# Kernel optimization log

Hardware: AMD Instinct MI355X
Metric: run time of the kernel (lower is better)

Reference implementation:

```python
import jax, jax.numpy as jnp
import numpy as np

N_NODES = 100000
N_EDGES = 1600000
D_IN, D_HID, D_OUT = 128, 256, 128


def _sage_conv(x, src, dst, W_l, b_l, W_r, num_nodes):
    """PyG SAGEConv with mean aggregation: lin_l(mean_j x_j) + lin_r(x_i)."""
    msg = x[src]                                              # [E, d] gather
    agg = jax.ops.segment_sum(msg, dst, num_segments=num_nodes)   # [N, d]
    cnt = jax.ops.segment_sum(jnp.ones((src.shape[0],), x.dtype), dst,
                              num_segments=num_nodes)         # [N]
    agg = agg / jnp.maximum(cnt, 1.0)[:, None]                # mean (0 for isolated)
    return agg @ W_l + b_l + x @ W_r


def setup_inputs() -> dict:
    key = jax.random.key(0)
    ks = jax.random.split(key, 8)
    x = jax.random.normal(ks[0], (N_NODES, D_IN), dtype=jnp.float32)
    edge_index = jax.random.randint(ks[1], (2, N_EDGES), 0, N_NODES, dtype=jnp.int64)
    perturb_first = jax.random.normal(ks[2], (N_NODES, D_HID), dtype=jnp.float32) * 0.05
    perturb_last = jax.random.normal(ks[3], (N_NODES, D_OUT), dtype=jnp.float32) * 0.05
    s1 = 1.0 / np.sqrt(D_IN)
    s2 = 1.0 / np.sqrt(D_HID)
    return {
        "x": x,
        "edge_index": edge_index,
        "perturb_first": perturb_first,
        "perturb_last": perturb_last,
        "Wl1": jax.random.normal(ks[4], (D_IN, D_HID), dtype=jnp.float32) * s1,
        "bl1": jnp.zeros((D_HID,), dtype=jnp.float32),
        "Wr1": jax.random.normal(ks[5], (D_IN, D_HID), dtype=jnp.float32) * s1,
        "Wl2": jax.random.normal(ks[6], (D_HID, D_OUT), dtype=jnp.float32) * s2,
        "bl2": jnp.zeros((D_OUT,), dtype=jnp.float32),
        "Wr2": jax.random.normal(ks[7], (D_HID, D_OUT), dtype=jnp.float32) * s2,
    }


def reference(x, edge_index, perturb_first, perturb_last,
              Wl1, bl1, Wr1, Wl2, bl2, Wr2):
    # PyG default flow source_to_target: messages from edge_index[0] -> edge_index[1]
    src, dst = edge_index[0], edge_index[1]
    n = x.shape[0]
    # forward() only applies model[0] and model[3] (the two SAGEConvs);
    # the LayerNorm/PReLU entries in the Sequential are skipped.
    h = _sage_conv(x, src, dst, Wl1, bl1, Wr1, n) + perturb_first
    out = _sage_conv(h, src, dst, Wl2, bl2, Wr2, n) + perturb_last
    return out
```

## Files before the change

### kernel.cpp

```cpp
#include <hip/hip_runtime.h>

#define N_NODES 100000
#define N_EDGES 1600000
#define NBUCK 196
#define CAP_BIN 64
#define CAP_B 12288
#define CVT_BLKS 12500

typedef float v4f __attribute__((ext_vector_type(4)));
typedef __bf16 v8bf __attribute__((ext_vector_type(8)));
typedef __bf16 v4bf __attribute__((ext_vector_type(4)));
typedef unsigned int v4u __attribute__((ext_vector_type(4)));

union FragU { v4u u; v8bf b; };
union PkU { unsigned int u; __bf16 h[2]; };
union Pk2 { uint2 u2; __bf16 h[4]; };

__device__ __forceinline__ int clampN(int v) {
    return v < 0 ? 0 : (v >= N_NODES ? N_NODES - 1 : v);
}
__device__ __forceinline__ float bfhi(unsigned int u) { return __uint_as_float(u & 0xffff0000u); }
__device__ __forceinline__ float bflo(unsigned int u) { return __uint_as_float(u << 16); }

__device__ __forceinline__ void gll16(const void* g, void* l) {
    __builtin_amdgcn_global_load_lds(
        (const __attribute__((address_space(1))) unsigned int*)g,
        (__attribute__((address_space(3))) unsigned int*)l, 16, 0, 0);
}

__global__ __launch_bounds__(256) void k_prep(
    const float* __restrict__ x, __bf16* __restrict__ a2,
    const float* __restrict__ Wl1, const float* __restrict__ Wr1,
    const float* __restrict__ Wl2, const float* __restrict__ Wr2,
    __bf16* __restrict__ Wl1p, __bf16* __restrict__ Wr1p,
    __bf16* __restrict__ Wl2p, __bf16* __restrict__ Wr2p,
    const int* __restrict__ dst, int* __restrict__ bucketCnt)
{
    const int b = blockIdx.x, tid = threadIdx.x;
    if (b < CVT_BLKS) {
        int t = b * 256 + tid;
        float4 v = ((const float4*)x)[t];
        int row = t >> 5, c4 = t & 31;
        v4bf o = { (__bf16)v.x, (__bf16)v.y, (__bf16)v.z, (__bf16)v.w };
        *(v4bf*)(a2 + (size_t)row * 256 + 128 + c4 * 4) = o;
    } else if (b < CVT_BLKS + 64) {
        int pb = b - CVT_BLKS;
        int which = pb >> 4;
        int t = (pb & 15) * 256 + tid;
        const float* W = which == 0 ? Wl1 : which == 1 ? Wr1 : which == 2 ? Wl2 : Wr2;
        __bf16* Wp     = which == 0 ? Wl1p : which == 1 ? Wr1p : which == 2 ? Wl2p : Wr2p;
        const int N = (which < 2) ? 256 : 128;
        const int NT = N >> 4;
        int l = t & 63;
        int fi = t >> 6;
        int kc = fi / NT, nt = fi % NT;
        int k0 = kc * 32 + (l >> 4) * 8;
        int col = nt * 16 + (l & 15);
        v8bf o;
        #pragma unroll
        for (int j = 0; j < 8; ++j) o[j] = (__bf16)W[(size_t)(k0 + j) * N + col];
        *(v8bf*)(Wp + (size_t)t * 8) = o;
    } else {
        __shared__ int h[NBUCK];
        for (int i = tid; i < NBUCK; i += 256) h[i] = 0;
        __syncthreads();
        int cb = b - CVT_BLKS - 64;
        int e0 = cb * 4096;
        int e1 = e0 + 4096; if (e1 > N_EDGES) e1 = N_EDGES;
        for (int e = e0 + tid; e < e1; e += 256)
            atomicAdd(&h[clampN(dst[e]) >> 9], 1);
        __syncthreads();
        for (int i = tid; i < NBUCK; i += 256)
            if (h[i]) atomicAdd(&bucketCnt[i], h[i]);
    }
}

__global__ __launch_bounds__(256) void k_scanb(
    const int* __restrict__ bucketCnt, int* __restrict__ baseB,
    int* __restrict__ gcur, int* __restrict__ rowp)
{
    const int t = threadIdx.x;
    int v = (t < NBUCK) ? bucketCnt[t] : 0;
    int incl = v;
    #pragma unroll
    for (int off = 1; off < 64; off <<= 1) {
        int u = __shfl_up(incl, off);
        if ((t & 63) >= off) incl += u;
    }
    __shared__ int wt[4];
    if ((t & 63) == 63) wt[t >> 6] = incl;
    __syncthreads();
    int woff = 0;
    #pragma unroll
    for (int k = 0; k < 4; ++k) if (k < (t >> 6)) woff += wt[k];
    int excl = woff + incl - v;
    if (t < NBUCK) { baseB[t] = excl; gcur[t] = excl; }
    if (t == NBUCK) { baseB[NBUCK] = excl; rowp[N_NODES] = excl; }
}

__global__ __launch_bounds__(256) void k_bin(
    const int* __restrict__ src, const int* __restrict__ dst,
    int* __restrict__ gcur, unsigned int* __restrict__ packed)
{
    __shared__ unsigned int bins[256 * CAP_BIN];
    __shared__ int cnt[256];
    const int tid = threadIdx.x;
    cnt[tid] = 0;
    __syncthreads();
    const int epb = (N_EDGES + gridDim.x - 1) / gridDim.x;
    int e0 = blockIdx.x * epb;
    int e1 = e0 + epb; if (e1 > N_EDGES) e1 = N_EDGES;
    for (int ch = e0; ch < e1; ch += 4096) {
        int chEnd = ch + 4096; if (chEnd > e1) chEnd = e1;
        for (int e = ch + tid; e < chEnd; e += 256) {
            int s = clampN(src[e]);
            int d = clampN(dst[e]);
            unsigned int val = (unsigned int)s | ((unsigned int)(d & 511) << 17);
            int b = d >> 9;
            int slot = atomicAdd(&cnt[b], 1);
            if (slot < CAP_BIN) bins[b * CAP_BIN + slot] = val;
            else {
                int g = atomicAdd(&gcur[b], 1);
                packed[g] = val;
            }
        }
        __syncthreads();
        int n = cnt[tid]; if (n > CAP_BIN) n = CAP_BIN;
        if (tid < NBUCK && n > 0) {
            int g = atomicAdd(&gcur[tid], n);
            for (int j = 0; j < n; ++j) packed[g + j] = bins[tid * CAP_BIN + j];
        }
        __syncthreads();
        cnt[tid] = 0;
        __syncthreads();
    }
}

__global__ __launch_bounds__(256) void k_bucket(
    const int* __restrict__ baseB, const unsigned int* __restrict__ packed,
    int* __restrict__ rowp, int* __restrict__ edge_src)
{
    __shared__ int hist[512], cur[512];
    __shared__ int wt[4];
    __shared__ unsigned int buf[CAP_B];
    const int b = blockIdx.x, tid = threadIdx.x;
    const int lo = baseB[b], hi = baseB[b + 1], c = hi - lo;
    for (int i = tid; i < 512; i += 256) hist[i] = 0;
    __syncthreads();
    for (int e = tid; e < c; e += 256)
        atomicAdd(&hist[packed[lo + e] >> 17], 1);
    __syncthreads();
    int a0 = hist[2 * tid], a1 = hist[2 * tid + 1];
    int s = a0 + a1;
    int incl = s;
    #pragma unroll
    for (int off = 1; off < 64; off <<= 1) {
        int u = __shfl_up(incl, off);
        if ((tid & 63) >= off) incl += u;
    }
    if ((tid & 63) == 63) wt[tid >> 6] = incl;
    __syncthreads();
    int woff = 0;
    #pragma unroll
    for (int k = 0; k < 4; ++k) if (k < (tid >> 6)) woff += wt[k];
    int ep = woff + incl - s;
    cur[2 * tid] = ep;
    cur[2 * tid + 1] = ep + a0;
    int n0 = b * 512 + 2 * tid;
    if (n0 < N_NODES)     rowp[n0]     = lo + ep;
    if (n0 + 1 < N_NODES) rowp[n0 + 1] = lo + ep + a0;
    __syncthreads();
    for (int e = tid; e < c; e += 256) {
        unsigned int v = packed[lo + e];
        int dl = v >> 17;
        unsigned int sv = v & 0x1FFFFu;
        int pos = atomicAdd(&cur[dl], 1);
        if (pos < CAP_B) buf[pos] = sv;
        else edge_src[lo + pos] = (int)sv;
    }
    __syncthreads();
    int cc = c < CAP_B ? c : CAP_B;
    for (int e = tid; e < cc; e += 256) edge_src[lo + e] = (int)buf[e];
}

template<int MODE>
__global__ __launch_bounds__(256) void k_gather16(
    const int* __restrict__ rp, const int* __restrict__ es,
    const __bf16* __restrict__ tab, void* __restrict__ outp)
{
    int wid = (blockIdx.x * 256 + threadIdx.x) >> 6;
    int l = threadIdx.x & 63;
    if (wid >= N_NODES) return;
    int start = rp[wid], end = rp[wid + 1];
    const int slot = l >> 4, c = l & 15;
    const size_t coff = (MODE == 0) ? (size_t)(128 + c * 8) : (size_t)(c * 8);
    float s0 = 0.f, s1 = 0.f, s2 = 0.f, s3 = 0.f;
    float s4 = 0.f, s5 = 0.f, s6 = 0.f, s7 = 0.f;

    int e0 = start + slot;
    int e1 = e0 + 4;
    int e2 = e1 + 4;
    bool h0 = e0 < end, h1 = e1 < end, h2 = e2 < end;
    v4u r0 = {0, 0, 0, 0}, r1 = {0, 0, 0, 0};
    if (h0) r0 = *(const v4u*)(tab + (size_t)es[e0] * 256 + coff);
    if (h1) r1 = *(const v4u*)(tab + (size_t)es[e1] * 256 + coff);
    int i2 = h2 ? es[e2] : 0;

    while (h0) {
        v4u r2 = {0, 0, 0, 0};
        if (h2) r2 = *(const v4u*)(tab + (size_t)i2 * 256 + coff);
        int e3 = e2 + 4;
        bool h3 = e3 < end;
        int i3 = h3 ? es[e3] : 0;
        s0 += bflo(r0.x); s1 += bfhi(r0.x);
        s2 += bflo(r0.y); s3 += bfhi(r0.y);
        s4 += bflo(r0.z); s5 += bfhi(r0.z);
        s6 += bflo(r0.w); s7 += bfhi(r0.w);
        r0 = r1; r1 = r2;
        h0 = h1; h1 = h2; h2 = h3;
        i2 = i3; e2 = e3;
    }

    s0 += __shfl_xor(s0, 16); s1 += __shfl_xor(s1, 16);
    s2 += __shfl_xor(s2, 16); s3 += __shfl_xor(s3, 16);
    s4 += __shfl_xor(s4, 16); s5 += __shfl_xor(s5, 16);
    s6 += __shfl_xor(s6, 16); s7 += __shfl_xor(s7, 16);
    s0 += __shfl_xor(s0, 32); s1 += __shfl_xor(s1, 32);
    s2 += __shfl_xor(s2, 32); s3 += __shfl_xor(s3, 32);
    s4 += __shfl_xor(s4, 32); s5 += __shfl_xor(s5, 32);
    s6 += __shfl_xor(s6, 32); s7 += __shfl_xor(s7, 32);
    float invd = 1.f / fmaxf((float)(end - start), 1.f);
    if (slot == 0) {
        if (MODE == 0) {
            PkU a, b, cc, d;
            a.h[0] = (__bf16)(s0 * invd); a.h[1] = (__bf16)(s1 * invd);
            b.h[0] = (__bf16)(s2 * invd); b.h[1] = (__bf16)(s3 * invd);
            cc.h[0] = (__bf16)(s4 * invd); cc.h[1] = (__bf16)(s5 * invd);
            d.h[0] = (__bf16)(s6 * invd); d.h[1] = (__bf16)(s7 * invd);
            v4u o = { a.u, b.u, cc.u, d.u };
            ((v4u*)outp)[(size_t)wid * 32 + c] = o;
        } else {
            v4u pu = *(const v4u*)(tab + (size_t)wid * 256 + 128 + c * 8);
            float4 va, vb;
            va.x = s0 * invd + bflo(pu.x); va.y = s1 * invd + bfhi(pu.x);
            va.z = s2 * invd + bflo(pu.y); va.w = s3 * invd + bfhi(pu.y);
            vb.x = s4 * invd + bflo(pu.z); vb.y = s5 * invd + bfhi(pu.z);
            vb.z = s6 * invd + bflo(pu.w); vb.w = s7 * invd + bfhi(pu.w);
            ((float4*)outp)[(size_t)wid * 32 + c * 2]     = va;
            ((float4*)outp)[(size_t)wid * 32 + c * 2 + 1] = vb;
        }
    }
}

template<int LAYER>
__device__ __forceinline__ void stage_a32(
    const __bf16* __restrict__ A, int tile, int tid, char* buf)
{
    const int row0 = tile * 32;
    #pragma unroll
    for (int k = 0; k < 2; ++k) {
        int ch = k * 512 + tid;
        int row = ch >> 5, c16 = ch & 31;
        int sc = c16 ^ (row & 7);
        gll16(A + (size_t)(row0 + row) * 256 + sc * 8, buf + ch * 16);
    }
}

template<int LAYER>
__device__ __forceinline__ void stage_p32(
    const float* __restrict__ pert, int tile, int tid, char* pS)
{
    const int row0 = tile * 32;
    if (LAYER == 1) {
        #pragma unroll
        for (int k = 0; k < 4; ++k) {
            int ch = k * 512 + tid;
            int row = ch >> 6, c16 = ch & 63;
            gll16(pert + (size_t)(row0 + row) * 256 + c16 * 4, pS + ch * 16);
        }
    } else {
        #pragma unroll
        for (int k = 0; k < 2; ++k) {
            int ch = k * 512 + tid;
            int row = ch >> 5, c16 = ch & 31;
            gll16(pert + (size_t)(row0 + row) * 128 + c16 * 4, pS + ch * 16);
        }
    }
}

template<int LAYER>
__global__ __launch_bounds__(512, 2) void k_gws(
    const __bf16* __restrict__ A,
    const __bf16* __restrict__ WpA, const __bf16* __restrict__ WpB,
    const float* __restrict__ bias, const float* __restrict__ pert,
    __bf16* __restrict__ outb, int ntiles)
{
    __shared__ char aS0[16384];
    __shared__ char aS1[16384];
    __shared__ char hS[16384];
    __shared__ char pS[(LAYER == 1) ? 32768 : 16384];
    const int tid = threadIdx.x;
    const int w = tid >> 6, l = tid & 63;
    const int lrow = l & 15, kg = l >> 4;
    const v4f zf = {0.f, 0.f, 0.f, 0.f};

    FragU bw[8][2];
    #pragma unroll
    for (int kc = 0; kc < 8; ++kc)
        #pragma unroll
        for (int nt = 0; nt < 2; ++nt) {
            const __bf16* Wp;
            int fi;
            if (LAYER == 1) {
                Wp = (kc < 4) ? WpA : WpB;
                fi = (kc & 3) * 16 + w * 2 + nt;
            } else {
                Wp = (w < 4) ? WpA : WpB;
                fi = kc * 8 + (w & 3) * 2 + nt;
            }
            bw[kc][nt].u = *(const v4u*)(Wp + ((size_t)fi * 64 + l) * 8);
        }

    int tile = blockIdx.x;
    int cur = 0;
    if (tile < ntiles) stage_a32<LAYER>(A, tile, tid, aS0);
    __syncthreads();

    for (; tile < ntiles; tile += gridDim.x) {
        stage_p32<LAYER>(pert, tile, tid, pS);
        int nxt = tile + (int)gridDim.x;
        if (nxt < ntiles)
            stage_a32<LAYER>(A, nxt, tid, cur ? aS0 : aS1);
        const char* aSc = cur ? aS1 : aS0;

        const int row0 = tile * 32;
        #pragma unroll
        for (int rf = 0; rf < 2; ++rf) {
            const int arow = rf * 16 + lrow;
            FragU a[8];
            #pragma unroll
            for (int kc = 0; kc < 8; ++kc) {
                int byte = arow * 512 + ((kc * 64 + kg * 16) ^ ((arow & 7) << 4));
                a[kc].u = *(const v4u*)(aSc + byte);
            }
            v4f acc[2] = {zf, zf};
            #pragma unroll
            for (int kc = 0; kc < 8; ++kc) {
                acc[0] = __builtin_amdgcn_mfma_f32_16x16x32_bf16(a[kc].b, bw[kc][0].b, acc[0], 0, 0, 0);
                acc[1] = __builtin_amdgcn_mfma_f32_16x16x32_bf16(a[kc].b, bw[kc][1].b, acc[1], 0, 0, 0);
            }
            #pragma unroll
            for (int nt = 0; nt < 2; ++nt)
                #pragma unroll
                for (int r = 0; r < 4; ++r) {
                    int row = rf * 16 + kg * 4 + r;
                    int col = w * 32 + nt * 16 + lrow;
                    int byte = (row * 512 + col * 2) ^ ((row & 7) << 4);
                    *(__bf16*)(hS + byte) = (__bf16)acc[nt][r];
                }
        }
        __syncthreads();

        #pragma unroll
        for (int it = 0; it < 4; ++it) {
            int chunk = it * 512 + tid;
            int row = chunk >> 6, c4 = chunk & 63;
            int grow = row0 + row;
            int byte = (row * 512 + c4 * 8) ^ ((row & 7) << 4);
            Pk2 pk; pk.u2 = *(const uint2*)(hS + byte);
            if (LAYER == 1) {
                float4 pv = *(const float4*)(pS + (row * 64 + c4) * 16);
                float4 bv = ((const float4*)bias)[c4];
                PkU o0, o1;
                o0.h[0] = (__bf16)((float)pk.h[0] + pv.x + bv.x);
                o0.h[1] = (__bf16)((float)pk.h[1] + pv.y + bv.y);
                o1.h[0] = (__bf16)((float)pk.h[2] + pv.z + bv.z);
                o1.h[1] = (__bf16)((float)pk.h[3] + pv.w + bv.w);
                uint2 ov = { o0.u, o1.u };
                *(uint2*)(outb + (size_t)grow * 256 + c4 * 4) = ov;
            } else {
                uint2 ov;
                if (c4 < 32) {
                    ov = pk.u2;
                } else {
                    float4 pv = *(const float4*)(pS + (row * 32 + (c4 - 32)) * 16);
                    float4 bv = ((const float4*)bias)[c4 - 32];
                    PkU o0, o1;
                    o0.h[0] = (__bf16)((float)pk.h[0] + pv.x + bv.x);
                    o0.h[1] = (__bf16)((float)pk.h[1] + pv.y + bv.y);
                    o1.h[0] = (__bf16)((float)pk.h[2] + pv.z + bv.z);
                    o1.h[1] = (__bf16)((float)pk.h[3] + pv.w + bv.w);
                    ov.x = o0.u; ov.y = o1.u;
                }
                *(uint2*)(outb + (size_t)grow * 256 + c4 * 4) = ov;
            }
        }
        __syncthreads();
        cur ^= 1;
    }
}

extern "C" void kernel_launch(void* const* d_in, const int* in_sizes, int n_in,
                              void* d_out, int out_size, void* d_ws, size_t ws_size,
                              hipStream_t stream)
{
    const float* x   = (const float*)d_in[0];
    const int*   ei  = (const int*)d_in[1];
    const float* p1  = (const float*)d_in[2];
    const float* p2  = (const float*)d_in[3];
    const float* Wl1 = (const float*)d_in[4];
    const float* bl1 = (const float*)d_in[5];
    const float* Wr1 = (const float*)d_in[6];
    const float* Wl2 = (const float*)d_in[7];
    const float* bl2 = (const float*)d_in[8];
    const float* Wr2 = (const float*)d_in[9];
    const int* src = ei;
    const int* dst = ei + N_EDGES;

    const size_t NPAD = (size_t)N_NODES + 64;
    char* wp = (char*)d_ws;
    __bf16* a2   = (__bf16*)wp; wp += NPAD * 256 * 2;
    __bf16* hb   = (__bf16*)wp; wp += NPAD * 256 * 2;
    __bf16* u2b  = (__bf16*)wp; wp += NPAD * 256 * 2;
    __bf16* Wl1p = (__bf16*)wp; wp += 128 * 256 * 2;
    __bf16* Wr1p = (__bf16*)wp; wp += 128 * 256 * 2;
    __bf16* Wl2p = (__bf16*)wp; wp += 256 * 128 * 2;
    __bf16* Wr2p = (__bf16*)wp; wp += 256 * 128 * 2;
    int* bucketCnt = (int*)wp; wp += 512 * 4;
    int* baseB     = (int*)wp; wp += 512 * 4;
    int* gcur      = (int*)wp; wp += 512 * 4;
    int* rowp      = (int*)wp; wp += (size_t)(N_NODES + 1) * 4 + 12;
    unsigned int* packed = (unsigned int*)wp; wp += (size_t)N_EDGES * 4;
    int* es        = (int*)wp;

    hipMemsetAsync(bucketCnt, 0, 512 * 4, stream);

    const int gblocks = (N_NODES * 64 + 255) / 256;
    const int tiles32 = N_NODES / 32;
    const int prep_blocks = CVT_BLKS + 64 + (N_EDGES + 4095) / 4096;

    k_prep<<<prep_blocks, 256, 0, stream>>>(
        x, a2, Wl1, Wr1, Wl2, Wr2, Wl1p, Wr1p, Wl2p, Wr2p, dst, bucketCnt);
    k_scanb<<<1, 256, 0, stream>>>(bucketCnt, baseB, gcur, rowp);
    k_bin<<<256, 256, 0, stream>>>(src, dst, gcur, packed);
    k_bucket<<<NBUCK, 256, 0, stream>>>(baseB, packed, rowp, es);

    k_gather16<0><<<gblocks, 256, 0, stream>>>(rowp, es, a2, a2);
    k_gws<1><<<512, 512, 0, stream>>>(a2, Wl1p, Wr1p, bl1, p1, hb, tiles32);
    k_gws<2><<<512, 512, 0, stream>>>(hb, Wl2p, Wr2p, bl2, p2, u2b, tiles32);
    k_gather16<1><<<gblocks, 256, 0, stream>>>(rowp, es, u2b, (void*)d_out);
}
```

Before: 289.4 us.

## Fuse layer-1 neighbor mean aggregation into the layer-1 GEMM kernel

The standalone layer-1 gather kernel is removed, and each 32-row tile of the layer-1 GEMM now gathers and averages its own neighbor rows straight into shared memory before running the MFMA products. This avoids writing the aggregated bf16 features to global memory and reading them back, and drops one kernel launch. In exchange, the GEMM kernel loses its double-buffered prefetch of A tiles. The irregular, latency-bound gather now runs inside a 512-thread, 2-blocks-per-CU kernel with only 512 blocks, which may lower memory-level parallelism for the gather.

New measurement: 378.1 us. 1.31x slower.

```diff
diff --git a/kernel.cpp b/kernel.cpp
--- a/kernel.cpp
+++ b/kernel.cpp
@@ -183,17 +183,16 @@
     for (int e = tid; e < cc; e += 256) edge_src[lo + e] = (int)buf[e];
 }
 
-template<int MODE>
-__global__ __launch_bounds__(256) void k_gather16(
+__global__ __launch_bounds__(256) void k_gather2(
     const int* __restrict__ rp, const int* __restrict__ es,
-    const __bf16* __restrict__ tab, void* __restrict__ outp)
+    const __bf16* __restrict__ tab, float* __restrict__ outp)
 {
     int wid = (blockIdx.x * 256 + threadIdx.x) >> 6;
     int l = threadIdx.x & 63;
     if (wid >= N_NODES) return;
     int start = rp[wid], end = rp[wid + 1];
     const int slot = l >> 4, c = l & 15;
-    const size_t coff = (MODE == 0) ? (size_t)(128 + c * 8) : (size_t)(c * 8);
+    const size_t coff = (size_t)(c * 8);
     float s0 = 0.f, s1 = 0.f, s2 = 0.f, s3 = 0.f;
     float s4 = 0.f, s5 = 0.f, s6 = 0.f, s7 = 0.f;
 
@@ -231,74 +230,28 @@
     s6 += __shfl_xor(s6, 32); s7 += __shfl_xor(s7, 32);
     float invd = 1.f / fmaxf((float)(end - start), 1.f);
     if (slot == 0) {
-        if (MODE == 0) {
-            PkU a, b, cc, d;
-            a.h[0] = (__bf16)(s0 * invd); a.h[1] = (__bf16)(s1 * invd);
-            b.h[0] = (__bf16)(s2 * invd); b.h[1] = (__bf16)(s3 * invd);
-            cc.h[0] = (__bf16)(s4 * invd); cc.h[1] = (__bf16)(s5 * invd);
-            d.h[0] = (__bf16)(s6 * invd); d.h[1] = (__bf16)(s7 * invd);
-            v4u o = { a.u, b.u, cc.u, d.u };
-            ((v4u*)outp)[(size_t)wid * 32 + c] = o;
-        } else {
-            v4u pu = *(const v4u*)(tab + (size_t)wid * 256 + 128 + c * 8);
-            float4 va, vb;
-            va.x = s0 * invd + bflo(pu.x); va.y = s1 * invd + bfhi(pu.x);
-            va.z = s2 * invd + bflo(pu.y); va.w = s3 * invd + bfhi(pu.y);
-            vb.x = s4 * invd + bflo(pu.z); vb.y = s5 * invd + bfhi(pu.z);
-            vb.z = s6 * invd + bflo(pu.w); vb.w = s7 * invd + bfhi(pu.w);
-            ((float4*)outp)[(size_t)wid * 32 + c * 2]     = va;
-            ((float4*)outp)[(size_t)wid * 32 + c * 2 + 1] = vb;
-        }
-    }
-}
-
-template<int LAYER>
-__device__ __forceinline__ void stage_a32(
-    const __bf16* __restrict__ A, int tile, int tid, char* buf)
-{
-    const int row0 = tile * 32;
-    #pragma unroll
-    for (int k = 0; k < 2; ++k) {
-        int ch = k * 512 + tid;
-        int row = ch >> 5, c16 = ch & 31;
-        int sc = c16 ^ (row & 7);
-        gll16(A + (size_t)(row0 + row) * 256 + sc * 8, buf + ch * 16);
-    }
-}
-
-template<int LAYER>
-__device__ __forceinline__ void stage_p32(
-    const float* __restrict__ pert, int tile, int tid, char* pS)
-{
-    const int row0 = tile * 32;
-    if (LAYER == 1) {
-        #pragma unroll
-        for (int k = 0; k < 4; ++k) {
-            int ch = k * 512 + tid;
-            int row = ch >> 6, c16 = ch & 63;
-            gll16(pert + (size_t)(row0 + row) * 256 + c16 * 4, pS + ch * 16);
-        }
-    } else {
-        #pragma unroll
-        for (int k = 0; k < 2; ++k) {
-            int ch = k * 512 + tid;
-            int row = ch >> 5, c16 = ch & 31;
-            gll16(pert + (size_t)(row0 + row) * 128 + c16 * 4, pS + ch * 16);
-        }
-    }
-}
-
-template<int LAYER>
-__global__ __launch_bounds__(512, 2) void k_gws(
-    const __bf16* __restrict__ A,
+        v4u pu = *(const v4u*)(tab + (size_t)wid * 256 + 128 + c * 8);
+        float4 va, vb;
+        va.x = s0 * invd + bflo(pu.x); va.y = s1 * invd + bfhi(pu.x);
+        va.z = s2 * invd + bflo(pu.y); va.w = s3 * invd + bfhi(pu.y);
+        vb.x = s4 * invd + bflo(pu.z); vb.y = s5 * invd + bfhi(pu.z);
+        vb.z = s6 * invd + bflo(pu.w); vb.w = s7 * invd + bfhi(pu.w);
+        ((float4*)outp)[(size_t)wid * 32 + c * 2]     = va;
+        ((float4*)outp)[(size_t)wid * 32 + c * 2 + 1] = vb;
+    }
+}
+
+__global__ __launch_bounds__(512, 2) void k_gws1g(
+    const __bf16* __restrict__ a2,
+    const int* __restrict__ rowp, const int* __restrict__ es,
     const __bf16* __restrict__ WpA, const __bf16* __restrict__ WpB,
     const float* __restrict__ bias, const float* __restrict__ pert,
     __bf16* __restrict__ outb, int ntiles)
 {
-    __shared__ char aS0[16384];
-    __shared__ char aS1[16384];
+    __shared__ char aAgg[8192];
+    __shared__ char aX[8192];
     __shared__ char hS[16384];
-    __shared__ char pS[(LAYER == 1) ? 32768 : 16384];
+    __shared__ char pS[32768];
     const int tid = threadIdx.x;
     const int w = tid >> 6, l = tid & 63;
     const int lrow = l & 15, kg = l >> 4;
@@ -309,39 +262,91 @@
     for (int kc = 0; kc < 8; ++kc)
         #pragma unroll
         for (int nt = 0; nt < 2; ++nt) {
-            const __bf16* Wp;
-            int fi;
-            if (LAYER == 1) {
-                Wp = (kc < 4) ? WpA : WpB;
-                fi = (kc & 3) * 16 + w * 2 + nt;
-            } else {
-                Wp = (w < 4) ? WpA : WpB;
-                fi = kc * 8 + (w & 3) * 2 + nt;
-            }
+            const __bf16* Wp = (kc < 4) ? WpA : WpB;
+            int fi = (kc & 3) * 16 + w * 2 + nt;
             bw[kc][nt].u = *(const v4u*)(Wp + ((size_t)fi * 64 + l) * 8);
         }
 
-    int tile = blockIdx.x;
-    int cur = 0;
-    if (tile < ntiles) stage_a32<LAYER>(A, tile, tid, aS0);
-    __syncthreads();
-
-    for (; tile < ntiles; tile += gridDim.x) {
-        stage_p32<LAYER>(pert, tile, tid, pS);
-        int nxt = tile + (int)gridDim.x;
-        if (nxt < ntiles)
-            stage_a32<LAYER>(A, nxt, tid, cur ? aS0 : aS1);
-        const char* aSc = cur ? aS1 : aS0;
-
+    const int slot = l >> 4, c = l & 15;
+
+    for (int tile = blockIdx.x; tile < ntiles; tile += gridDim.x) {
         const int row0 = tile * 32;
+        {
+            int row = tid >> 4, ci = tid & 15;
+            int sc = ci ^ (row & 7);
+            gll16(a2 + (size_t)(row0 + row) * 256 + 128 + sc * 8, aX + tid * 16);
+        }
+        #pragma unroll
+        for (int k2 = 0; k2 < 4; ++k2) {
+            int ch = k2 * 512 + tid;
+            int row = ch >> 6, c16 = ch & 63;
+            gll16(pert + (size_t)(row0 + row) * 256 + c16 * 4, pS + ch * 16);
+        }
+
+        #pragma unroll
+        for (int j = 0; j < 4; ++j) {
+            const int row = w * 4 + j;
+            const int grow = row0 + row;
+            int start = rowp[grow], end = rowp[grow + 1];
+            float s0 = 0.f, s1 = 0.f, s2 = 0.f, s3 = 0.f;
+            float s4 = 0.f, s5 = 0.f, s6 = 0.f, s7 = 0.f;
+            int e0 = start + slot;
+            int e1 = e0 + 4;
+            int e2 = e1 + 4;
+            bool h0 = e0 < end, h1 = e1 < end, h2 = e2 < end;
+            v4u r0 = {0, 0, 0, 0}, r1 = {0, 0, 0, 0};
+            if (h0) r0 = *(const v4u*)(a2 + (size_t)es[e0] * 256 + 128 + c * 8);
+            if (h1) r1 = *(const v4u*)(a2 + (size_t)es[e1] * 256 + 128 + c * 8);
+            int i2 = h2 ? es[e2] : 0;
+            while (h0) {
+                v4u r2 = {0, 0, 0, 0};
+                if (h2) r2 = *(const v4u*)(a2 + (size_t)i2 * 256 + 128 + c * 8);
+                int e3 = e2 + 4;
+                bool h3 = e3 < end;
+                int i3 = h3 ? es[e3] : 0;
+                s0 += bflo(r0.x); s1 += bfhi(r0.x);
+                s2 += bflo(r0.y); s3 += bfhi(r0.y);
+                s4 += bflo(r0.z); s5 += bfhi(r0.z);
+                s6 += bflo(r0.w); s7 += bfhi(r0.w);
+                r0 = r1; r1 = r2;
+                h0 = h1; h1 = h2; h2 = h3;
+                i2 = i3; e2 = e3;
+            }
+            s0 += __shfl_xor(s0, 16); s1 += __shfl_xor(s1, 16);
+            s2 += __shfl_xor(s2, 16); s3 += __shfl_xor(s3, 16);
+            s4 += __shfl_xor(s4, 16); s5 += __shfl_xor(s5, 16);
+            s6 += __shfl_xor(s6, 16); s7 += __shfl_xor(s7, 16);
+            s0 += __shfl_xor(s0, 32); s1 += __shfl_xor(s1, 32);
+            s2 += __shfl_xor(s2, 32); s3 += __shfl_xor(s3, 32);
+            s4 += __shfl_xor(s4, 32); s5 += __shfl_xor(s5, 32);
+            s6 += __shfl_xor(s6, 32); s7 += __shfl_xor(s7, 32);
+            float invd = 1.f / fmaxf((float)(end - start), 1.f);
+            if (slot == 0) {
+                PkU pa, pb, pc, pd;
+                pa.h[0] = (__bf16)(s0 * invd); pa.h[1] = (__bf16)(s1 * invd);
+                pb.h[0] = (__bf16)(s2 * invd); pb.h[1] = (__bf16)(s3 * invd);
+                pc.h[0] = (__bf16)(s4 * invd); pc.h[1] = (__bf16)(s5 * invd);
+                pd.h[0] = (__bf16)(s6 * invd); pd.h[1] = (__bf16)(s7 * invd);
+                v4u o = { pa.u, pb.u, pc.u, pd.u };
+                int byte = row * 256 + ((c * 16) ^ ((row & 7) << 4));
+                *(v4u*)(aAgg + byte) = o;
+            }
+        }
+        __syncthreads();
+
         #pragma unroll
         for (int rf = 0; rf < 2; ++rf) {
             const int arow = rf * 16 + lrow;
             FragU a[8];
             #pragma unroll
-            for (int kc = 0; kc < 8; ++kc) {
-                int byte = arow * 512 + ((kc * 64 + kg * 16) ^ ((arow & 7) << 4));
-                a[kc].u = *(const v4u*)(aSc + byte);
+            for (int kc = 0; kc < 4; ++kc) {
+                int byte = arow * 256 + ((kc * 64 + kg * 16) ^ ((arow & 7) << 4));
+                a[kc].u = *(const v4u*)(aAgg + byte);
+            }
+            #pragma unroll
+            for (int kc = 4; kc < 8; ++kc) {
+                int byte = arow * 256 + (((kc - 4) * 64 + kg * 16) ^ ((arow & 7) << 4));
+                a[kc].u = *(const v4u*)(aX + byte);
             }
             v4f acc[2] = {zf, zf};
             #pragma unroll
@@ -368,32 +373,125 @@
             int grow = row0 + row;
             int byte = (row * 512 + c4 * 8) ^ ((row & 7) << 4);
             Pk2 pk; pk.u2 = *(const uint2*)(hS + byte);
-            if (LAYER == 1) {
-                float4 pv = *(const float4*)(pS + (row * 64 + c4) * 16);
-                float4 bv = ((const float4*)bias)[c4];
+            float4 pv = *(const float4*)(pS + (row * 64 + c4) * 16);
+            float4 bv = ((const float4*)bias)[c4];
+            PkU o0, o1;
+            o0.h[0] = (__bf16)((float)pk.h[0] + pv.x + bv.x);
+            o0.h[1] = (__bf16)((float)pk.h[1] + pv.y + bv.y);
+            o1.h[0] = (__bf16)((float)pk.h[2] + pv.z + bv.z);
+            o1.h[1] = (__bf16)((float)pk.h[3] + pv.w + bv.w);
+            uint2 ov = { o0.u, o1.u };
+            *(uint2*)(outb + (size_t)grow * 256 + c4 * 4) = ov;
+        }
+        __syncthreads();
+    }
+}
+
+__device__ __forceinline__ void stage_a32(
+    const __bf16* __restrict__ A, int tile, int tid, char* buf)
+{
+    const int row0 = tile * 32;
+    #pragma unroll
+    for (int k = 0; k < 2; ++k) {
+        int ch = k * 512 + tid;
+        int row = ch >> 5, c16 = ch & 31;
+        int sc = c16 ^ (row & 7);
+        gll16(A + (size_t)(row0 + row) * 256 + sc * 8, buf + ch * 16);
+    }
+}
+
+__global__ __launch_bounds__(512, 2) void k_gws2(
+    const __bf16* __restrict__ A,
+    const __bf16* __restrict__ WpA, const __bf16* __restrict__ WpB,
+    const float* __restrict__ bias, const float* __restrict__ pert,
+    __bf16* __restrict__ outb, int ntiles)
+{
+    __shared__ char aS0[16384];
+    __shared__ char aS1[16384];
+    __shared__ char hS[16384];
+    __shared__ char pS[16384];
+    const int tid = threadIdx.x;
+    const int w = tid >> 6, l = tid & 63;
+    const int lrow = l & 15, kg = l >> 4;
+    const v4f zf = {0.f, 0.f, 0.f, 0.f};
+
+    FragU bw[8][2];
+    #pragma unroll
+    for (int kc = 0; kc < 8; ++kc)
+        #pragma unroll
+        for (int nt = 0; nt < 2; ++nt) {
+            const __bf16* Wp = (w < 4) ? WpA : WpB;
+            int fi = kc * 8 + (w & 3) * 2 + nt;
+            bw[kc][nt].u = *(const v4u*)(Wp + ((size_t)fi * 64 + l) * 8);
+        }
+
+    int tile = blockIdx.x;
+    int cur = 0;
+    if (tile < ntiles) stage_a32(A, tile, tid, aS0);
+    __syncthreads();
+
+    for (; tile < ntiles; tile += gridDim.x) {
+        {
+            #pragma unroll
+            for (int k = 0; k < 2; ++k) {
+                int ch = k * 512 + tid;
+                int row = ch >> 5, c16 = ch & 31;
+                gll16(pert + (size_t)(tile * 32 + row) * 128 + c16 * 4, pS + ch * 16);
+            }
+        }
+        int nxt = tile + (int)gridDim.x;
+        if (nxt < ntiles) stage_a32(A, nxt, tid, cur ? aS0 : aS1);
+        const char* aSc = cur ? aS1 : aS0;
+
+        const int row0 = tile * 32;
+        #pragma unroll
+        for (int rf = 0; rf < 2; ++rf) {
+            const int arow = rf * 16 + lrow;
+            FragU a[8];
+            #pragma unroll
+            for (int kc = 0; kc < 8; ++kc) {
+                int byte = arow * 512 + ((kc * 64 + kg * 16) ^ ((arow & 7) << 4));
+                a[kc].u = *(const v4u*)(aSc + byte);
+            }
+            v4f acc[2] = {zf, zf};
+            #pragma unroll
+            for (int kc = 0; kc < 8; ++kc) {
+                acc[0] = __builtin_amdgcn_mfma_f32_16x16x32_bf16(a[kc].b, bw[kc][0].b, acc[0], 0, 0, 0);
+                acc[1] = __builtin_amdgcn_mfma_f32_16x16x32_bf16(a[kc].b, bw[kc][1].b, acc[1], 0, 0, 0);
+            }
+            #pragma unroll
+            for (int nt = 0; nt < 2; ++nt)
+                #pragma unroll
+                for (int r = 0; r < 4; ++r) {
+                    int row = rf * 16 + kg * 4 + r;
+                    int col = w * 32 + nt * 16 + lrow;
+                    int byte = (row * 512 + col * 2) ^ ((row & 7) << 4);
+                    *(__bf16*)(hS + byte) = (__bf16)acc[nt][r];
+                }
+        }
+        __syncthreads();
+
+        #pragma unroll
+        for (int it = 0; it < 4; ++it) {
+            int chunk = it * 512 + tid;
+            int row = chunk >> 6, c4 = chunk & 63;
+            int grow = row0 + row;
+            int byte = (row * 512 + c4 * 8) ^ ((row & 7) << 4);
+            Pk2 pk; pk.u2 = *(const uint2*)(hS + byte);
+            uint2 ov;
+            if (c4 < 32) {
+                ov = pk.u2;
+            } else {
+                float4 pv = *(const float4*)(pS + (row * 32 + (c4 - 32)) * 16);
+                float4 bv = ((const float4*)bias)[c4 - 32];
                 PkU o0, o1;
                 o0.h[0] = (__bf16)((float)pk.h[0] + pv.x + bv.x);
                 o0.h[1] = (__bf16)((float)pk.h[1] + pv.y + bv.y);
                 o1.h[0] = (__bf16)((float)pk.h[2] + pv.z + bv.z);
                 o1.h[1] = (__bf16)((float)pk.h[3] + pv.w + bv.w);
-                uint2 ov = { o0.u, o1.u };
-                *(uint2*)(outb + (size_t)grow * 256 + c4 * 4) = ov;
-            } else {
-                uint2 ov;
-                if (c4 < 32) {
-                    ov = pk.u2;
-                } else {
-                    float4 pv = *(const float4*)(pS + (row * 32 + (c4 - 32)) * 16);
-                    float4 bv = ((const float4*)bias)[c4 - 32];
-                    PkU o0, o1;
-                    o0.h[0] = (__bf16)((float)pk.h[0] + pv.x + bv.x);
-                    o0.h[1] = (__bf16)((float)pk.h[1] + pv.y + bv.y);
-                    o1.h[0] = (__bf16)((float)pk.h[2] + pv.z + bv.z);
-                    o1.h[1] = (__bf16)((float)pk.h[3] + pv.w + bv.w);
-                    ov.x = o0.u; ov.y = o1.u;
-                }
-                *(uint2*)(outb + (size_t)grow * 256 + c4 * 4) = ov;
-            }
+                ov.x = o0.u; ov.y = o1.u;
+            }
+            *(uint2*)(outb + (size_t)grow * 256 + c4 * 4) = ov;
         }
         __syncthreads();
         cur ^= 1;
@@ -445,8 +543,7 @@
     k_bin<<<256, 256, 0, stream>>>(src, dst, gcur, packed);
     k_bucket<<<NBUCK, 256, 0, stream>>>(baseB, packed, rowp, es);
 
-    k_gather16<0><<<gblocks, 256, 0, stream>>>(rowp, es, a2, a2);
-    k_gws<1><<<512, 512, 0, stream>>>(a2, Wl1p, Wr1p, bl1, p1, hb, tiles32);
-    k_gws<2><<<512, 512, 0, stream>>>(hb, Wl2p, Wr2p, bl2, p2, u2b, tiles32);
-    k_gather16<1><<<gblocks, 256, 0, stream>>>(rowp, es, u2b, (void*)d_out);
-}
+    k_gws1g<<<512, 512, 0, stream>>>(a2, rowp, es, Wl1p, Wr1p, bl1, p1, hb, tiles32);
+    k_gws2<<<512, 512, 0, stream>>>(hb, Wl2p, Wr2p, bl2, p2, u2b, tiles32);
+    k_gather2<<<gblocks, 256, 0, stream>>>(rowp, es, u2b, (float*)d_out);
+}
```
